# Kernel optimization log

Measured on AMD Instinct MI355X. Metric: run time of the kernel, lower is better.

## Reference

```python
import jax, jax.numpy as jnp
import numpy as np

LIMIT = 7.0      # self.m.limit
ACT_ALPHA = 1.702  # self.m.alpha (GLU sigmoid slope)
R = 8
LORA_ALPHA = 16.0
SCALING = LORA_ALPHA / R
E, H, F = 8, 2048, 1024
D = 2 * F
B, S, K = 2, 1024, 4


def setup_inputs() -> dict:
    key = jax.random.key(0)
    ks = jax.random.split(key, 12)
    w = 0.02  # realistic weight scale
    return {
        "hidden_states": jax.random.normal(ks[0], (B, S, H), jnp.float32),
        "routing_weights": jax.random.uniform(ks[1], (B * S, K), jnp.float32),
        "gate_up_proj": jax.random.normal(ks[2], (E, H, D), jnp.float32) * w,
        "gate_up_proj_bias": jax.random.normal(ks[3], (E, D), jnp.float32) * w,
        "down_proj": jax.random.normal(ks[4], (E, F, H), jnp.float32) * w,
        "down_proj_bias": jax.random.normal(ks[5], (E, H), jnp.float32) * w,
        "lora_gate_up_A": jax.random.normal(ks[6], (E, H, R), jnp.float32) * w,
        "lora_gate_up_B": jax.random.normal(ks[7], (E, R, D), jnp.float32) * w,
        "lora_down_A": jax.random.normal(ks[8], (E, F, R), jnp.float32) * w,
        "lora_down_B": jax.random.normal(ks[9], (E, R, H), jnp.float32) * w,
        "router_indices": jax.random.randint(ks[10], (B * S, K), 0, E, jnp.int64),
    }


def reference(hidden_states, routing_weights, gate_up_proj, gate_up_proj_bias,
              down_proj, down_proj_bias, lora_gate_up_A, lora_gate_up_B,
              lora_down_A, lora_down_B, router_indices):
    b, s, h = hidden_states.shape
    x = hidden_states.reshape(-1, h)  # [T,H]
    # Combined per-(expert,token) routing weight: sum over top-k slots that hit expert e.
    onehot = jax.nn.one_hot(router_indices, E, dtype=x.dtype)        # [T,K,E]
    w = jnp.einsum('tke,tk->et', onehot, routing_weights)            # [E,T]
    # gate_up projection with inline LoRA (per expert, all tokens; masked by w later)
    lora1 = jnp.einsum('etr,erd->etd', jnp.einsum('th,ehr->etr', x, lora_gate_up_A), lora_gate_up_B)
    gate_up = jnp.einsum('th,ehd->etd', x, gate_up_proj) + SCALING * lora1 + gate_up_proj_bias[:, None, :]
    gate = jnp.minimum(gate_up[..., ::2], LIMIT)                     # [E,T,F]
    up = jnp.clip(gate_up[..., 1::2], -LIMIT, LIMIT)
    glu = gate * jax.nn.sigmoid(gate * ACT_ALPHA)
    gated = (up + 1.0) * glu                                         # [E,T,F]
    # down projection with inline LoRA
    lora2 = jnp.einsum('etr,erh->eth', jnp.einsum('etf,efr->etr', gated, lora_down_A), lora_down_B)
    out = jnp.einsum('etf,efh->eth', gated, down_proj) + SCALING * lora2 + down_proj_bias[:, None, :]
    # scatter-combine: weight each expert output and sum over experts
    next_states = jnp.einsum('et,eth->th', w, out)                   # [T,H]
    return next_states.reshape(b, s, h)
```

## Files before the change

### kernel.cpp

```cpp
#include <hip/hip_runtime.h>
#include <stdint.h>


typedef short bf16x8 __attribute__((ext_vector_type(8)));
typedef float f32x4 __attribute__((ext_vector_type(4)));

__device__ __forceinline__ short bf16r(float f) {
  uint32_t u = __float_as_uint(f);
  u += 0x7fffu + ((u >> 16) & 1u);
  return (short)(u >> 16);
}

__device__ __forceinline__ float bf16f(short s) {
  uint32_t u = ((uint32_t)(uint16_t)s) << 16;
  return __uint_as_float(u);
}

__device__ __forceinline__ void load_lds16(const void* g, void* l) {
  __builtin_amdgcn_global_load_lds((const __attribute__((address_space(1))) void*)g,
                                   (__attribute__((address_space(3))) void*)l,
                                   16, 0, 0);
}

__global__ void k_route(const int* __restrict__ idx_raw, const float* __restrict__ rw,
                        float* __restrict__ w, int* __restrict__ cnt, int* __restrict__ list,
                        int* __restrict__ tok_nh, int* __restrict__ tok_pair) {
  __shared__ int s_nz;
  const int tid = threadIdx.x;
  if (tid == 0) s_nz = 0;
  __syncthreads();
  int found = 0;
  for (int i = tid; i < 4096; i += 256) found |= idx_raw[2 * i + 1];
  if (found) atomicOr(&s_nz, 1);
  __syncthreads();
  const bool is64 = (s_nz == 0);

  const int t = blockIdx.x * 256 + tid;
  int ek[4]; float rk[4];
#pragma unroll
  for (int k = 0; k < 4; k++) {
    ek[k] = is64 ? idx_raw[2 * (t * 4 + k)] : idx_raw[t * 4 + k];
    rk[k] = rw[t * 4 + k];
  }
  int j = 0;
#pragma unroll
  for (int e = 0; e < 8; e++) {
    float s = 0.f;
#pragma unroll
    for (int k = 0; k < 4; k++) s += (ek[k] == e) ? rk[k] : 0.f;
    w[e * 2048 + t] = s;
    if (s != 0.f) {
      int slot = atomicAdd(&cnt[e], 1);
      list[e * 2048 + slot] = t;
      tok_pair[t * 4 + j] = (e << 16) | slot;
      j++;
    }
  }
  tok_nh[t] = j;
}

__global__ void k_prefix(const int* __restrict__ cnt, int* __restrict__ offs) {
  if (threadIdx.x == 0 && blockIdx.x == 0) {
    int s = 0;
    for (int e = 0; e < 8; e++) { offs[e] = s; s += cnt[e]; }
    offs[8] = s;
  }
}

__global__ void k_wprep(const float* __restrict__ W, const float* __restrict__ A,
                        const float* __restrict__ Bm, short* __restrict__ O,
                        int Kd, int Nd) {
  const int e = blockIdx.z;
  const float* We = W + (size_t)e * Kd * Nd;
  const float* Ae = A + (size_t)e * Kd * 8;
  const float* Be = Bm + (size_t)e * 8 * Nd;
  short* Oe = O + (size_t)e * Kd * Nd;
  __shared__ float tile[64][33];
  __shared__ float As[64][9];
  __shared__ float Bs[8][32];
  const int n0 = blockIdx.x * 32, k0 = blockIdx.y * 64;
  const int tx = threadIdx.x & 31, ty = threadIdx.x >> 5;
#pragma unroll
  for (int i = 0; i < 8; i++)
    tile[ty + 8 * i][tx] = We[(size_t)(k0 + ty + 8 * i) * Nd + n0 + tx];
  {
    int kk = threadIdx.x >> 3, r = threadIdx.x & 7;
    As[kk][r] = Ae[(size_t)(k0 + kk) * 8 + r];
    As[kk + 32][r] = Ae[(size_t)(k0 + kk + 32) * 8 + r];
  }
  {
    int rr = threadIdx.x >> 5, nn = threadIdx.x & 31;
    Bs[rr][nn] = Be[(size_t)rr * Nd + n0 + nn];
  }
  __syncthreads();
  const int kk2 = threadIdx.x & 63, ng = threadIdx.x >> 6;
#pragma unroll
  for (int i = 0; i < 8; i++) {
    int n = ng + 4 * i;
    float v = tile[kk2][n];
    float l = 0.f;
#pragma unroll
    for (int r = 0; r < 8; r++) l += As[kk2][r] * Bs[r][n];
    Oe[(size_t)(n0 + n) * Kd + k0 + kk2] = bf16r(v + 2.0f * l);
  }
}

__global__ void k_xconv(const float* __restrict__ x, short* __restrict__ xb) {
  const int i = (blockIdx.x * 256 + threadIdx.x) * 4;
  float4 v = *(const float4*)(x + i);
  short4 s;
  s.x = bf16r(v.x); s.y = bf16r(v.y); s.z = bf16r(v.z); s.w = bf16r(v.w);
  *(short4*)(xb + i) = s;
}


#define PH_SYNC() do { \
    asm volatile("s_barrier" ::: "memory"); \
    asm volatile("s_waitcnt lgkmcnt(0)" ::: "memory"); \
    __builtin_amdgcn_sched_barrier(0); \
    __builtin_amdgcn_s_setprio(1); } while (0)
#define PH_END() do { \
    __builtin_amdgcn_s_setprio(0); \
    asm volatile("s_barrier" ::: "memory"); } while (0)
#define PH_END_GATE() do { \
    __builtin_amdgcn_s_setprio(0); \
    asm volatile("s_waitcnt vmcnt(4)" ::: "memory"); \
    asm volatile("s_barrier" ::: "memory"); } while (0)

#define MM(AARR, BARR, MG, NG) \
  _Pragma("unroll") \
  for (int f_ = 0; f_ < 4; ++f_) \
    _Pragma("unroll") \
    for (int g_ = 0; g_ < 2; ++g_) \
      _Pragma("unroll") \
      for (int s_ = 0; s_ < 2; ++s_) \
        acc[(MG) + f_][(NG) + g_] = __builtin_amdgcn_mfma_f32_16x16x32_bf16( \
            AARR[f_][s_], BARR[g_][s_], acc[(MG) + f_][(NG) + g_], 0, 0, 0);

template <int KDIM, bool GATHER, bool GLU>
__global__ __launch_bounds__(512) void k_gemm8p(
    const short* __restrict__ Abuf, const short* __restrict__ Bbuf,
    const float* __restrict__ bias, const int* __restrict__ cnt,
    const int* __restrict__ offs, const int* __restrict__ list,
    short* __restrict__ outbuf) {
  constexpr int KT = KDIM / 64;
  constexpr int NIT = KT / 2;
  const int e = blockIdx.z;
  const int M = cnt[e];
  const int m0 = blockIdx.y * 256;
  if (m0 >= M) return;
  const int n0 = blockIdx.x * 256;
  const int off_e = offs[e];
  const short* Bp = Bbuf + (size_t)e * 2048 * KDIM;

  __shared__ __align__(16) short sA[2 * 256 * 64];
  __shared__ __align__(16) short sB[2 * 256 * 64];
  constexpr int SLOT = 256 * 64;
  constexpr int HALF = 128 * 64;

  const int tid = threadIdx.x;
  const int lane = tid & 63;
  const int wv = tid >> 6;
  const int wr = wv >> 2;
  const int wc = wv & 3;
  const int lm = lane & 15;
  const int quad = lane >> 4;

  const int srow = tid >> 3;
  const int scol = ((tid & 7) ^ (srow & 7)) * 8;
  uint32_t offA[4], offB[4];
#pragma unroll
  for (int j = 0; j < 4; ++j) {
    const int r = m0 + srow + 64 * j;
    const int rc = min(r, M - 1);
    if constexpr (GATHER) {
      offA[j] = (uint32_t)list[e * 2048 + rc] * (uint32_t)KDIM + (uint32_t)scol;
    } else {
      offA[j] = (uint32_t)(off_e + rc) * (uint32_t)KDIM + (uint32_t)scol;
    }
    offB[j] = (uint32_t)(n0 + srow + 64 * j) * (uint32_t)KDIM + (uint32_t)scol;
  }

  auto stageA = [&](int slot, int h, int kt) {
    short* d = sA + slot * SLOT + h * HALF + tid * 8;
    load_lds16(Abuf + offA[2 * h] + kt * 64, d);
    load_lds16(Abuf + offA[2 * h + 1] + kt * 64, d + 4096);
  };
  auto stageB = [&](int slot, int h, int kt) {
    short* d = sB + slot * SLOT + h * HALF + tid * 8;
    load_lds16(Bp + offB[2 * h] + kt * 64, d);
    load_lds16(Bp + offB[2 * h + 1] + kt * 64, d + 4096);
  };

  const int rbA = (wr * 128 + lm) * 64;
  const int rbB = (wc * 64 + lm) * 64;
  const int c0 = ((0 + quad) ^ (lane & 7)) * 8;
  const int c1 = ((4 + quad) ^ (lane & 7)) * 8;

  auto rdA = [&](int slot, int mg, bf16x8 (&a)[4][2]) {
#pragma unroll
    for (int f = 0; f < 4; ++f) {
      const short* p = sA + slot * SLOT + rbA + (mg + f) * 1024;
      a[f][0] = *(const bf16x8*)(p + c0);
      a[f][1] = *(const bf16x8*)(p + c1);
    }
  };
  auto rdB = [&](int slot, int ng, bf16x8 (&b)[2][2]) {
#pragma unroll
    for (int g = 0; g < 2; ++g) {
      const short* p = sB + slot * SLOT + rbB + (ng + g) * 1024;
      b[g][0] = *(const bf16x8*)(p + c0);
      b[g][1] = *(const bf16x8*)(p + c1);
    }
  };

  f32x4 acc[8][4];
#pragma unroll
  for (int i = 0; i < 8; ++i)
#pragma unroll
    for (int j = 0; j < 4; ++j) acc[i][j] = (f32x4){0.f, 0.f, 0.f, 0.f};

  stageB(0, 0, 0); stageB(0, 1, 0);
  stageA(0, 0, 0); stageA(0, 1, 0);
  {
    const int k1 = (1 < KT - 1) ? 1 : (KT - 1);
    stageB(1, 0, k1); stageB(1, 1, k1);
  }
  asm volatile("s_waitcnt vmcnt(4)" ::: "memory");
  asm volatile("s_barrier" ::: "memory");

  bf16x8 aLo[4][2], aHi[4][2], bLo[2][2], bHi[2][2];

#pragma unroll 1
  for (int it = 0; it < NIT; ++it) {
    const int tb = 2 * it + 1;
    const int tS0 = min(2 * it + 2, KT - 1);
    const int tS1 = min(2 * it + 3, KT - 1);
    rdA(0, 0, aLo); rdB(0, 0, bLo);
    stageA(1, 0, tb);
    PH_SYNC(); MM(aLo, bLo, 0, 0); PH_END();
    rdB(0, 2, bHi);
    stageA(1, 1, tb);
    PH_SYNC(); MM(aLo, bHi, 0, 2); PH_END();
    rdA(0, 4, aHi);
    stageB(0, 0, tS0);
    PH_SYNC(); MM(aHi, bLo, 4, 0); PH_END();
    stageB(0, 1, tS0);
    PH_SYNC(); MM(aHi, bHi, 4, 2); PH_END_GATE();
    rdA(1, 0, aLo); rdB(1, 0, bLo);
    stageA(0, 0, tS0);
    PH_SYNC(); MM(aLo, bLo, 0, 0); PH_END();
    rdB(1, 2, bHi);
    stageA(0, 1, tS0);
    PH_SYNC(); MM(aLo, bHi, 0, 2); PH_END();
    rdA(1, 4, aHi);
    stageB(1, 0, tS1);
    PH_SYNC(); MM(aHi, bLo, 4, 0); PH_END();
    stageB(1, 1, tS1);
    PH_SYNC(); MM(aHi, bHi, 4, 2); PH_END_GATE();
  }

  if constexpr (GLU) {
    const float* be = bias + e * 2048;
#pragma unroll
    for (int m = 0; m < 8; ++m) {
      const int rbase = m0 + wr * 128 + m * 16 + quad * 4;
#pragma unroll
      for (int g = 0; g < 4; ++g) {
        const int col = n0 + wc * 64 + g * 16 + lm;
        const float bb = be[col];
#pragma unroll
        for (int r = 0; r < 4; ++r) {
          const int slot = rbase + r;
          float val = acc[m][g][r] + bb;
          float other = __shfl_xor(val, 1);
          if (((lane & 1) == 0) && (slot < M)) {
            float gt = fminf(val, 7.f);
            float u = fminf(fmaxf(other, -7.f), 7.f);
            float glu = gt / (1.f + __expf(-1.702f * gt));
            outbuf[(size_t)(off_e + slot) * 1024 + (col >> 1)] = bf16r((u + 1.f) * glu);
          }
        }
      }
    }
  } else {
#pragma unroll
    for (int m = 0; m < 8; ++m) {
#pragma unroll
      for (int r = 0; r < 4; ++r) {
        const int slot = m0 + wr * 128 + m * 16 + quad * 4 + r;
        if (slot >= M) continue;
        short* prow = outbuf + (size_t)(off_e + slot) * 2048;
#pragma unroll
        for (int g = 0; g < 4; ++g) {
          const int h = n0 + wc * 64 + g * 16 + lm;
          prow[h] = bf16r(acc[m][g][r]);
        }
      }
    }
  }
}

__global__ __launch_bounds__(256) void k_combine(
    const short* __restrict__ pairbuf, const float* __restrict__ bias2,
    const float* __restrict__ wbuf, const int* __restrict__ offs,
    const int* __restrict__ tok_nh, const int* __restrict__ tok_pair,
    float* __restrict__ out) {
  const int t = blockIdx.x;
  const int h0 = threadIdx.x * 8;
  const int nh = tok_nh[t];
  float acc[8];
#pragma unroll
  for (int i = 0; i < 8; i++) acc[i] = 0.f;
  for (int j = 0; j < nh; j++) {
    const int p = tok_pair[t * 4 + j];
    const int e = p >> 16, slot = p & 0xffff;
    const float wt = wbuf[e * 2048 + t];
    const bf16x8 v = *(const bf16x8*)(pairbuf + (size_t)(offs[e] + slot) * 2048 + h0);
    const float4 bA = *(const float4*)(bias2 + e * 2048 + h0);
    const float4 bB = *(const float4*)(bias2 + e * 2048 + h0 + 4);
    acc[0] += wt * (bf16f(v[0]) + bA.x);
    acc[1] += wt * (bf16f(v[1]) + bA.y);
    acc[2] += wt * (bf16f(v[2]) + bA.z);
    acc[3] += wt * (bf16f(v[3]) + bA.w);
    acc[4] += wt * (bf16f(v[4]) + bB.x);
    acc[5] += wt * (bf16f(v[5]) + bB.y);
    acc[6] += wt * (bf16f(v[6]) + bB.z);
    acc[7] += wt * (bf16f(v[7]) + bB.w);
  }
  float4 oA = {acc[0], acc[1], acc[2], acc[3]};
  float4 oB = {acc[4], acc[5], acc[6], acc[7]};
  *(float4*)(out + (size_t)t * 2048 + h0) = oA;
  *(float4*)(out + (size_t)t * 2048 + h0 + 4) = oB;
}

extern "C" void kernel_launch(void* const* d_in, const int* in_sizes, int n_in,
                              void* d_out, int out_size, void* d_ws, size_t ws_size,
                              hipStream_t stream) {
  const float* x   = (const float*)d_in[0];
  const float* rw  = (const float*)d_in[1];
  const float* w1  = (const float*)d_in[2];
  const float* b1  = (const float*)d_in[3];
  const float* w2  = (const float*)d_in[4];
  const float* b2  = (const float*)d_in[5];
  const float* a1  = (const float*)d_in[6];
  const float* lb1 = (const float*)d_in[7];
  const float* a2  = (const float*)d_in[8];
  const float* lb2 = (const float*)d_in[9];
  const int* idx   = (const int*)d_in[10];
  float* out = (float*)d_out;

  char* ws = (char*)d_ws;
  int* cnt     = (int*)(ws);
  int* offs    = (int*)(ws + 64);
  int* tok_nh  = (int*)(ws + 128);
  float* wbuf  = (float*)(ws + 16384);
  int* list    = (int*)(ws + 81920);
  int* tok_pair= (int*)(ws + 147456);
  short* Xb    = (short*)(ws + (1ull << 20));
  short* gated = (short*)(ws + 9437184ull);
  short* W2T   = (short*)(ws + 26214400ull);
  short* W1T   = (short*)(ws + 59768832ull);
  short* pairbuf = (short*)(ws + 59768832ull);

  hipMemsetAsync(cnt, 0, 64, stream);

  k_route<<<dim3(8), dim3(256), 0, stream>>>(idx, rw, wbuf, cnt, list, tok_nh, tok_pair);
  k_prefix<<<dim3(1), dim3(64), 0, stream>>>(cnt, offs);
  k_wprep<<<dim3(64, 32, 8), dim3(256), 0, stream>>>(w1, a1, lb1, W1T, 2048, 2048);
  k_wprep<<<dim3(64, 16, 8), dim3(256), 0, stream>>>(w2, a2, lb2, W2T, 1024, 2048);
  k_xconv<<<dim3(4096), dim3(256), 0, stream>>>(x, Xb);
  k_gemm8p<2048, true, true><<<dim3(8, 8, 8), dim3(512), 0, stream>>>(
      Xb, W1T, b1, cnt, offs, list, gated);
  k_gemm8p<1024, false, false><<<dim3(8, 8, 8), dim3(512), 0, stream>>>(
      gated, W2T, nullptr, cnt, offs, nullptr, pairbuf);
  k_combine<<<dim3(2048), dim3(256), 0, stream>>>(pairbuf, b2, wbuf, offs, tok_nh, tok_pair, out);
}
```

Baseline: 432.9 us.

## Schedule expert GEMM tiles from a compacted work list in a persistent grid

k_prefix now builds a compact list of valid (expert, m-tile, n-tile) items, ordered round-robin across experts, and records the item count. Both grouped GEMMs launch a 1D grid of 256 blocks that loop over this list, replacing the 8x8x8 grid where blocks past an expert's token count exited immediately. The aim is to avoid launching empty blocks and to spread experts' tiles evenly across CUs. The cost is a serial list build on one thread and a per-item loop with re-initialised addressing state.

Result: no change. 440.1 us (+1.7%).

```diff
diff --git a/kernel.cpp b/kernel.cpp
--- a/kernel.cpp
+++ b/kernel.cpp
@@ -59,11 +59,20 @@
   tok_nh[t] = j;
 }
 
-__global__ void k_prefix(const int* __restrict__ cnt, int* __restrict__ offs) {
+__global__ void k_prefix(const int* __restrict__ cnt, int* __restrict__ offs,
+                         int* __restrict__ wl) {
   if (threadIdx.x == 0 && blockIdx.x == 0) {
-    int s = 0;
-    for (int e = 0; e < 8; e++) { offs[e] = s; s += cnt[e]; }
+    int s = 0; int nb[8];
+    for (int e = 0; e < 8; e++) {
+      offs[e] = s; s += cnt[e];
+      nb[e] = (cnt[e] + 255) >> 8;
+    }
     offs[8] = s;
+    int p = 0;
+    for (int j = 0; j < 64; j++)
+      for (int e = 0; e < 8; e++)
+        if (j < nb[e] * 8) wl[p++] = (e << 6) | j;
+    offs[9] = p;
   }
 }
 
@@ -141,17 +150,10 @@
 __global__ __launch_bounds__(512) void k_gemm8p(
     const short* __restrict__ Abuf, const short* __restrict__ Bbuf,
     const float* __restrict__ bias, const int* __restrict__ cnt,
-    const int* __restrict__ offs, const int* __restrict__ list,
-    short* __restrict__ outbuf) {
+    const int* __restrict__ offs, const int* __restrict__ wl,
+    const int* __restrict__ list, short* __restrict__ outbuf) {
   constexpr int KT = KDIM / 64;
   constexpr int NIT = KT / 2;
-  const int e = blockIdx.z;
-  const int M = cnt[e];
-  const int m0 = blockIdx.y * 256;
-  if (m0 >= M) return;
-  const int n0 = blockIdx.x * 256;
-  const int off_e = offs[e];
-  const short* Bp = Bbuf + (size_t)e * 2048 * KDIM;
 
   __shared__ __align__(16) short sA[2 * 256 * 64];
   __shared__ __align__(16) short sB[2 * 256 * 64];
@@ -168,133 +170,146 @@
 
   const int srow = tid >> 3;
   const int scol = ((tid & 7) ^ (srow & 7)) * 8;
-  uint32_t offA[4], offB[4];
-#pragma unroll
-  for (int j = 0; j < 4; ++j) {
-    const int r = m0 + srow + 64 * j;
-    const int rc = min(r, M - 1);
-    if constexpr (GATHER) {
-      offA[j] = (uint32_t)list[e * 2048 + rc] * (uint32_t)KDIM + (uint32_t)scol;
-    } else {
-      offA[j] = (uint32_t)(off_e + rc) * (uint32_t)KDIM + (uint32_t)scol;
-    }
-    offB[j] = (uint32_t)(n0 + srow + 64 * j) * (uint32_t)KDIM + (uint32_t)scol;
-  }
-
-  auto stageA = [&](int slot, int h, int kt) {
-    short* d = sA + slot * SLOT + h * HALF + tid * 8;
-    load_lds16(Abuf + offA[2 * h] + kt * 64, d);
-    load_lds16(Abuf + offA[2 * h + 1] + kt * 64, d + 4096);
-  };
-  auto stageB = [&](int slot, int h, int kt) {
-    short* d = sB + slot * SLOT + h * HALF + tid * 8;
-    load_lds16(Bp + offB[2 * h] + kt * 64, d);
-    load_lds16(Bp + offB[2 * h + 1] + kt * 64, d + 4096);
-  };
 
   const int rbA = (wr * 128 + lm) * 64;
   const int rbB = (wc * 64 + lm) * 64;
   const int c0 = ((0 + quad) ^ (lane & 7)) * 8;
   const int c1 = ((4 + quad) ^ (lane & 7)) * 8;
 
-  auto rdA = [&](int slot, int mg, bf16x8 (&a)[4][2]) {
-#pragma unroll
-    for (int f = 0; f < 4; ++f) {
-      const short* p = sA + slot * SLOT + rbA + (mg + f) * 1024;
-      a[f][0] = *(const bf16x8*)(p + c0);
-      a[f][1] = *(const bf16x8*)(p + c1);
-    }
-  };
-  auto rdB = [&](int slot, int ng, bf16x8 (&b)[2][2]) {
-#pragma unroll
-    for (int g = 0; g < 2; ++g) {
-      const short* p = sB + slot * SLOT + rbB + (ng + g) * 1024;
-      b[g][0] = *(const bf16x8*)(p + c0);
-      b[g][1] = *(const bf16x8*)(p + c1);
-    }
-  };
-
-  f32x4 acc[8][4];
-#pragma unroll
-  for (int i = 0; i < 8; ++i)
-#pragma unroll
-    for (int j = 0; j < 4; ++j) acc[i][j] = (f32x4){0.f, 0.f, 0.f, 0.f};
-
-  stageB(0, 0, 0); stageB(0, 1, 0);
-  stageA(0, 0, 0); stageA(0, 1, 0);
-  {
-    const int k1 = (1 < KT - 1) ? 1 : (KT - 1);
-    stageB(1, 0, k1); stageB(1, 1, k1);
-  }
-  asm volatile("s_waitcnt vmcnt(4)" ::: "memory");
-  asm volatile("s_barrier" ::: "memory");
-
-  bf16x8 aLo[4][2], aHi[4][2], bLo[2][2], bHi[2][2];
+  const int nitems = offs[9];
+
+  for (int item = blockIdx.x; item < nitems; item += 256) {
+    const int wit = wl[item];
+    const int e = wit >> 6;
+    const int m0 = ((wit >> 3) & 7) * 256;
+    const int n0 = (wit & 7) * 256;
+    const int M = cnt[e];
+    const int off_e = offs[e];
+    const short* Bp = Bbuf + (size_t)e * 2048 * KDIM;
+
+    uint32_t offA[4], offB[4];
+#pragma unroll
+    for (int j = 0; j < 4; ++j) {
+      const int r = m0 + srow + 64 * j;
+      const int rc = min(r, M - 1);
+      if constexpr (GATHER) {
+        offA[j] = (uint32_t)list[e * 2048 + rc] * (uint32_t)KDIM + (uint32_t)scol;
+      } else {
+        offA[j] = (uint32_t)(off_e + rc) * (uint32_t)KDIM + (uint32_t)scol;
+      }
+      offB[j] = (uint32_t)(n0 + srow + 64 * j) * (uint32_t)KDIM + (uint32_t)scol;
+    }
+
+    auto stageA = [&](int slot, int h, int kt) {
+      short* d = sA + slot * SLOT + h * HALF + tid * 8;
+      load_lds16(Abuf + offA[2 * h] + kt * 64, d);
+      load_lds16(Abuf + offA[2 * h + 1] + kt * 64, d + 4096);
+    };
+    auto stageB = [&](int slot, int h, int kt) {
+      short* d = sB + slot * SLOT + h * HALF + tid * 8;
+      load_lds16(Bp + offB[2 * h] + kt * 64, d);
+      load_lds16(Bp + offB[2 * h + 1] + kt * 64, d + 4096);
+    };
+
+    auto rdA = [&](int slot, int mg, bf16x8 (&a)[4][2]) {
+#pragma unroll
+      for (int f = 0; f < 4; ++f) {
+        const short* p = sA + slot * SLOT + rbA + (mg + f) * 1024;
+        a[f][0] = *(const bf16x8*)(p + c0);
+        a[f][1] = *(const bf16x8*)(p + c1);
+      }
+    };
+    auto rdB = [&](int slot, int ng, bf16x8 (&b)[2][2]) {
+#pragma unroll
+      for (int g = 0; g < 2; ++g) {
+        const short* p = sB + slot * SLOT + rbB + (ng + g) * 1024;
+        b[g][0] = *(const bf16x8*)(p + c0);
+        b[g][1] = *(const bf16x8*)(p + c1);
+      }
+    };
+
+    f32x4 acc[8][4];
+#pragma unroll
+    for (int i = 0; i < 8; ++i)
+#pragma unroll
+      for (int j = 0; j < 4; ++j) acc[i][j] = (f32x4){0.f, 0.f, 0.f, 0.f};
+
+    stageB(0, 0, 0); stageB(0, 1, 0);
+    stageA(0, 0, 0); stageA(0, 1, 0);
+    {
+      const int k1 = (1 < KT - 1) ? 1 : (KT - 1);
+      stageB(1, 0, k1); stageB(1, 1, k1);
+    }
+    asm volatile("s_waitcnt vmcnt(4)" ::: "memory");
+    asm volatile("s_barrier" ::: "memory");
+
+    bf16x8 aLo[4][2], aHi[4][2], bLo[2][2], bHi[2][2];
 
 #pragma unroll 1
-  for (int it = 0; it < NIT; ++it) {
-    const int tb = 2 * it + 1;
-    const int tS0 = min(2 * it + 2, KT - 1);
-    const int tS1 = min(2 * it + 3, KT - 1);
-    rdA(0, 0, aLo); rdB(0, 0, bLo);
-    stageA(1, 0, tb);
-    PH_SYNC(); MM(aLo, bLo, 0, 0); PH_END();
-    rdB(0, 2, bHi);
-    stageA(1, 1, tb);
-    PH_SYNC(); MM(aLo, bHi, 0, 2); PH_END();
-    rdA(0, 4, aHi);
-    stageB(0, 0, tS0);
-    PH_SYNC(); MM(aHi, bLo, 4, 0); PH_END();
-    stageB(0, 1, tS0);
-    PH_SYNC(); MM(aHi, bHi, 4, 2); PH_END_GATE();
-    rdA(1, 0, aLo); rdB(1, 0, bLo);
-    stageA(0, 0, tS0);
-    PH_SYNC(); MM(aLo, bLo, 0, 0); PH_END();
-    rdB(1, 2, bHi);
-    stageA(0, 1, tS0);
-    PH_SYNC(); MM(aLo, bHi, 0, 2); PH_END();
-    rdA(1, 4, aHi);
-    stageB(1, 0, tS1);
-    PH_SYNC(); MM(aHi, bLo, 4, 0); PH_END();
-    stageB(1, 1, tS1);
-    PH_SYNC(); MM(aHi, bHi, 4, 2); PH_END_GATE();
-  }
-
-  if constexpr (GLU) {
-    const float* be = bias + e * 2048;
-#pragma unroll
-    for (int m = 0; m < 8; ++m) {
-      const int rbase = m0 + wr * 128 + m * 16 + quad * 4;
-#pragma unroll
-      for (int g = 0; g < 4; ++g) {
-        const int col = n0 + wc * 64 + g * 16 + lm;
-        const float bb = be[col];
-#pragma unroll
-        for (int r = 0; r < 4; ++r) {
-          const int slot = rbase + r;
-          float val = acc[m][g][r] + bb;
-          float other = __shfl_xor(val, 1);
-          if (((lane & 1) == 0) && (slot < M)) {
-            float gt = fminf(val, 7.f);
-            float u = fminf(fmaxf(other, -7.f), 7.f);
-            float glu = gt / (1.f + __expf(-1.702f * gt));
-            outbuf[(size_t)(off_e + slot) * 1024 + (col >> 1)] = bf16r((u + 1.f) * glu);
+    for (int it = 0; it < NIT; ++it) {
+      const int tb = 2 * it + 1;
+      const int tS0 = min(2 * it + 2, KT - 1);
+      const int tS1 = min(2 * it + 3, KT - 1);
+      rdA(0, 0, aLo); rdB(0, 0, bLo);
+      stageA(1, 0, tb);
+      PH_SYNC(); MM(aLo, bLo, 0, 0); PH_END();
+      rdB(0, 2, bHi);
+      stageA(1, 1, tb);
+      PH_SYNC(); MM(aLo, bHi, 0, 2); PH_END();
+      rdA(0, 4, aHi);
+      stageB(0, 0, tS0);
+      PH_SYNC(); MM(aHi, bLo, 4, 0); PH_END();
+      stageB(0, 1, tS0);
+      PH_SYNC(); MM(aHi, bHi, 4, 2); PH_END_GATE();
+      rdA(1, 0, aLo); rdB(1, 0, bLo);
+      stageA(0, 0, tS0);
+      PH_SYNC(); MM(aLo, bLo, 0, 0); PH_END();
+      rdB(1, 2, bHi);
+      stageA(0, 1, tS0);
+      PH_SYNC(); MM(aLo, bHi, 0, 2); PH_END();
+      rdA(1, 4, aHi);
+      stageB(1, 0, tS1);
+      PH_SYNC(); MM(aHi, bLo, 4, 0); PH_END();
+      stageB(1, 1, tS1);
+      PH_SYNC(); MM(aHi, bHi, 4, 2); PH_END_GATE();
+    }
+
+    if constexpr (GLU) {
+      const float* be = bias + e * 2048;
+#pragma unroll
+      for (int m = 0; m < 8; ++m) {
+        const int rbase = m0 + wr * 128 + m * 16 + quad * 4;
+#pragma unroll
+        for (int g = 0; g < 4; ++g) {
+          const int col = n0 + wc * 64 + g * 16 + lm;
+          const float bb = be[col];
+#pragma unroll
+          for (int r = 0; r < 4; ++r) {
+            const int slot = rbase + r;
+            float val = acc[m][g][r] + bb;
+            float other = __shfl_xor(val, 1);
+            if (((lane & 1) == 0) && (slot < M)) {
+              float gt = fminf(val, 7.f);
+              float u = fminf(fmaxf(other, -7.f), 7.f);
+              float glu = gt / (1.f + __expf(-1.702f * gt));
+              outbuf[(size_t)(off_e + slot) * 1024 + (col >> 1)] = bf16r((u + 1.f) * glu);
+            }
           }
         }
       }
-    }
-  } else {
-#pragma unroll
-    for (int m = 0; m < 8; ++m) {
-#pragma unroll
-      for (int r = 0; r < 4; ++r) {
-        const int slot = m0 + wr * 128 + m * 16 + quad * 4 + r;
-        if (slot >= M) continue;
-        short* prow = outbuf + (size_t)(off_e + slot) * 2048;
-#pragma unroll
-        for (int g = 0; g < 4; ++g) {
-          const int h = n0 + wc * 64 + g * 16 + lm;
-          prow[h] = bf16r(acc[m][g][r]);
+    } else {
+#pragma unroll
+      for (int m = 0; m < 8; ++m) {
+#pragma unroll
+        for (int r = 0; r < 4; ++r) {
+          const int slot = m0 + wr * 128 + m * 16 + quad * 4 + r;
+          if (slot >= M) continue;
+          short* prow = outbuf + (size_t)(off_e + slot) * 2048;
+#pragma unroll
+          for (int g = 0; g < 4; ++g) {
+            const int h = n0 + wc * 64 + g * 16 + lm;
+            prow[h] = bf16r(acc[m][g][r]);
+          }
         }
       }
     }
@@ -354,6 +369,7 @@
   int* cnt     = (int*)(ws);
   int* offs    = (int*)(ws + 64);
   int* tok_nh  = (int*)(ws + 128);
+  int* wl      = (int*)(ws + 8320);
   float* wbuf  = (float*)(ws + 16384);
   int* list    = (int*)(ws + 81920);
   int* tok_pair= (int*)(ws + 147456);
@@ -366,13 +382,13 @@
   hipMemsetAsync(cnt, 0, 64, stream);
 
   k_route<<<dim3(8), dim3(256), 0, stream>>>(idx, rw, wbuf, cnt, list, tok_nh, tok_pair);
-  k_prefix<<<dim3(1), dim3(64), 0, stream>>>(cnt, offs);
+  k_prefix<<<dim3(1), dim3(64), 0, stream>>>(cnt, offs, wl);
   k_wprep<<<dim3(64, 32, 8), dim3(256), 0, stream>>>(w1, a1, lb1, W1T, 2048, 2048);
   k_wprep<<<dim3(64, 16, 8), dim3(256), 0, stream>>>(w2, a2, lb2, W2T, 1024, 2048);
   k_xconv<<<dim3(4096), dim3(256), 0, stream>>>(x, Xb);
-  k_gemm8p<2048, true, true><<<dim3(8, 8, 8), dim3(512), 0, stream>>>(
-      Xb, W1T, b1, cnt, offs, list, gated);
-  k_gemm8p<1024, false, false><<<dim3(8, 8, 8), dim3(512), 0, stream>>>(
-      gated, W2T, nullptr, cnt, offs, nullptr, pairbuf);
+  k_gemm8p<2048, true, true><<<dim3(256), dim3(512), 0, stream>>>(
+      Xb, W1T, b1, cnt, offs, wl, list, gated);
+  k_gemm8p<1024, false, false><<<dim3(256), dim3(512), 0, stream>>>(
+      gated, W2T, nullptr, cnt, offs, wl, nullptr, pairbuf);
   k_combine<<<dim3(2048), dim3(256), 0, stream>>>(pairbuf, b2, wbuf, offs, tok_nh, tok_pair, out);
 }
```
